# Kernel tuning notes

Hardware: AMD Instinct MI355X
Metric: run time of the kernel (lower is better)

The kernel has to match this reference:

```python
import jax, jax.numpy as jnp
import numpy as np

E = 1024
H = 16
D = E // H
B = 32
S = 1024


def _layernorm(x, gamma, beta, eps=1e-5):
    mu = jnp.mean(x, axis=-1, keepdims=True)
    var = jnp.var(x, axis=-1, keepdims=True)
    return (x - mu) * jax.lax.rsqrt(var + eps) * gamma + beta


def setup_inputs() -> dict:
    key = jax.random.key(0)
    ks = jax.random.split(key, 16)
    w = lambda k, shape: jax.random.normal(k, shape, dtype=jnp.float32) * 0.02
    return {
        "img_feat": jax.random.normal(ks[0], (B, S, E), dtype=jnp.float32),
        "heat_feat": jax.random.normal(ks[1], (B, E), dtype=jnp.float32),
        "W_img": w(ks[2], (E, E)), "b_img": jnp.zeros((E,), jnp.float32),
        "W_heat": w(ks[3], (E, E)), "b_heat": jnp.zeros((E,), jnp.float32),
        "Wq": w(ks[4], (E, E)), "bq": jnp.zeros((E,), jnp.float32),
        "Wk": w(ks[5], (E, E)), "bk": jnp.zeros((E,), jnp.float32),
        "Wv": w(ks[6], (E, E)), "bv": jnp.zeros((E,), jnp.float32),
        "Wo": w(ks[7], (E, E)), "bo": jnp.zeros((E,), jnp.float32),
        "gamma": jnp.ones((E,), jnp.float32),
        "beta": jnp.zeros((E,), jnp.float32),
    }


def reference(img_feat, heat_feat, W_img, b_img, W_heat, b_heat,
              Wq, bq, Wk, bk, Wv, bv, Wo, bo, gamma, beta):
    # projections (torch Linear: x @ W.T + b)
    proj_heat = (heat_feat @ W_heat.T + b_heat)[:, None, :]        # [B,1,E]
    proj_img = img_feat @ W_img.T + b_img                          # [B,S,E]
    # multi-head attention, KV seq len = 1
    q = (proj_img @ Wq.T + bq).reshape(B, S, H, D)
    k = (proj_heat @ Wk.T + bk).reshape(B, 1, H, D)
    v = (proj_heat @ Wv.T + bv).reshape(B, 1, H, D)
    scale = 1.0 / np.sqrt(D).astype(np.float32)
    scores = jnp.einsum('bshd,bthd->bhst', q, k) * scale           # [B,H,S,1]
    attn = jax.nn.softmax(scores, axis=-1)                         # == ones
    ctx = jnp.einsum('bhst,bthd->bshd', attn, v).reshape(B, S, E)
    attn_out = ctx @ Wo.T + bo                                     # [B,S,E]
    # residual + LayerNorm (dropout is identity in eval)
    return _layernorm(img_feat + attn_out, gamma, beta)
```

## Files before the change

kernel.cpp:

```cpp
#include <hip/hip_runtime.h>


#define E_DIM 1024
#define B_DIM 32
#define S_DIM 1024

__global__ __launch_bounds__(256) void gemv_f32(
        const float* __restrict__ W,
        const float* __restrict__ bias,
        const float* __restrict__ x,
        float* __restrict__ y) {
    int wave = threadIdx.x >> 6;
    int lane = threadIdx.x & 63;
    int out_idx = (blockIdx.x << 2) + wave;
    int b = out_idx >> 10;
    int e = out_idx & (E_DIM - 1);
    const float4* w4 = reinterpret_cast<const float4*>(W + (size_t)e * E_DIM);
    const float4* x4 = reinterpret_cast<const float4*>(x + (size_t)b * E_DIM);
    float acc = 0.f;
    #pragma unroll
    for (int p = 0; p < 4; ++p) {
        float4 wv = w4[p * 64 + lane];
        float4 xv = x4[p * 64 + lane];
        acc += wv.x * xv.x + wv.y * xv.y + wv.z * xv.z + wv.w * xv.w;
    }
    #pragma unroll
    for (int off = 32; off; off >>= 1)
        acc += __shfl_down(acc, off, 64);
    if (lane == 0) y[out_idx] = acc + bias[e];
}

__global__ __launch_bounds__(256) void resid_layernorm(
        const float* __restrict__ img,
        const float* __restrict__ a,
        const float* __restrict__ gamma,
        const float* __restrict__ beta,
        float* __restrict__ out) {
    const int row = blockIdx.x;
    const int b = row >> 10;
    const int t = threadIdx.x;

    const float4* imgp = reinterpret_cast<const float4*>(img + (size_t)row * E_DIM);
    const float4* ap   = reinterpret_cast<const float4*>(a + (size_t)b * E_DIM);

    float4 iv = imgp[t];
    float4 av = ap[t];

    float x0 = iv.x + av.x;
    float x1 = iv.y + av.y;
    float x2 = iv.z + av.z;
    float x3 = iv.w + av.w;

    float s = x0 + x1 + x2 + x3;
    float q = x0 * x0 + x1 * x1 + x2 * x2 + x3 * x3;

    #pragma unroll
    for (int off = 32; off; off >>= 1) {
        s += __shfl_down(s, off, 64);
        q += __shfl_down(q, off, 64);
    }

    __shared__ float ssum[4], sqq[4];
    int wv = t >> 6, ln = t & 63;
    if (ln == 0) { ssum[wv] = s; sqq[wv] = q; }
    __syncthreads();
    if (t == 0) {
        float S = ssum[0] + ssum[1] + ssum[2] + ssum[3];
        float Q = sqq[0] + sqq[1] + sqq[2] + sqq[3];
        float mu = S * (1.0f / E_DIM);
        float var = Q * (1.0f / E_DIM) - mu * mu;
        ssum[0] = mu;
        sqq[0] = rsqrtf(var + 1e-5f);
    }
    __syncthreads();
    float mu = ssum[0];
    float rstd = sqq[0];

    const float4* gp = reinterpret_cast<const float4*>(gamma) + t;
    const float4* bp = reinterpret_cast<const float4*>(beta) + t;
    float4 gv = *gp, bv = *bp;

    float4 ov;
    ov.x = (x0 - mu) * rstd * gv.x + bv.x;
    ov.y = (x1 - mu) * rstd * gv.y + bv.y;
    ov.z = (x2 - mu) * rstd * gv.z + bv.z;
    ov.w = (x3 - mu) * rstd * gv.w + bv.w;

    reinterpret_cast<float4*>(out + (size_t)row * E_DIM)[t] = ov;
}

extern "C" void kernel_launch(void* const* d_in, const int* in_sizes, int n_in,
                              void* d_out, int out_size, void* d_ws, size_t ws_size,
                              hipStream_t stream) {
    const float* heat   = (const float*)d_in[1];
    const float* W_heat = (const float*)d_in[4];
    const float* b_heat = (const float*)d_in[5];
    const float* Wv     = (const float*)d_in[10];
    const float* bvv    = (const float*)d_in[11];
    const float* Wo     = (const float*)d_in[12];
    const float* bo     = (const float*)d_in[13];
    const float* img    = (const float*)d_in[0];
    const float* gamma  = (const float*)d_in[14];
    const float* beta   = (const float*)d_in[15];
    float* out = (float*)d_out;

    float* ws = (float*)d_ws;
    float* tt = ws;
    float* vv = ws + B_DIM * E_DIM;
    float* aa = ws + 2 * B_DIM * E_DIM;

    const int n_be = B_DIM * E_DIM;
    const int gemv_blocks = n_be / 4;

    gemv_f32<<<gemv_blocks, 256, 0, stream>>>(W_heat, b_heat, heat, tt);
    gemv_f32<<<gemv_blocks, 256, 0, stream>>>(Wv, bvv, tt, vv);
    gemv_f32<<<gemv_blocks, 256, 0, stream>>>(Wo, bo, vv, aa);

    resid_layernorm<<<B_DIM * S_DIM, 256, 0, stream>>>(img, aa, gamma, beta, out);
}
```

Measured before the change: 295.0 us.

## Reuse weight rows across batches in GEMV and process multiple LayerNorm rows per wave

```diff
diff --git a/kernel.cpp b/kernel.cpp
--- a/kernel.cpp
+++ b/kernel.cpp
@@ -5,88 +5,125 @@
 #define B_DIM 32
 #define S_DIM 1024
 
-__global__ __launch_bounds__(256) void gemv_f32(
+__global__ __launch_bounds__(256) void gemv_xlds(
         const float* __restrict__ W,
         const float* __restrict__ bias,
         const float* __restrict__ x,
         float* __restrict__ y) {
-    int wave = threadIdx.x >> 6;
-    int lane = threadIdx.x & 63;
-    int out_idx = (blockIdx.x << 2) + wave;
-    int b = out_idx >> 10;
-    int e = out_idx & (E_DIM - 1);
+    __shared__ float4 xs[8 * 256];
+    const int t = threadIdx.x;
+    const int rg = blockIdx.x & 255;
+    const int bq = blockIdx.x >> 8;
+
+    const float4* x4 = reinterpret_cast<const float4*>(x) + (size_t)bq * 8 * 256;
+    #pragma unroll
+    for (int i = 0; i < 8; ++i)
+        xs[i * 256 + t] = x4[i * 256 + t];
+    __syncthreads();
+
+    const int wave = t >> 6;
+    const int lane = t & 63;
+    const int e = rg * 4 + wave;
+
     const float4* w4 = reinterpret_cast<const float4*>(W + (size_t)e * E_DIM);
-    const float4* x4 = reinterpret_cast<const float4*>(x + (size_t)b * E_DIM);
-    float acc = 0.f;
+    float4 w0 = w4[lane];
+    float4 w1 = w4[64 + lane];
+    float4 w2 = w4[128 + lane];
+    float4 w3 = w4[192 + lane];
+
+    float acc[8];
     #pragma unroll
-    for (int p = 0; p < 4; ++p) {
-        float4 wv = w4[p * 64 + lane];
-        float4 xv = x4[p * 64 + lane];
-        acc += wv.x * xv.x + wv.y * xv.y + wv.z * xv.z + wv.w * xv.w;
+    for (int i = 0; i < 8; ++i) acc[i] = 0.f;
+
+    #pragma unroll
+    for (int i = 0; i < 8; ++i) {
+        float4 a0 = xs[i * 256 + lane];
+        float4 a1 = xs[i * 256 + 64 + lane];
+        float4 a2 = xs[i * 256 + 128 + lane];
+        float4 a3 = xs[i * 256 + 192 + lane];
+        float r = w0.x * a0.x + w0.y * a0.y + w0.z * a0.z + w0.w * a0.w;
+        r += w1.x * a1.x + w1.y * a1.y + w1.z * a1.z + w1.w * a1.w;
+        r += w2.x * a2.x + w2.y * a2.y + w2.z * a2.z + w2.w * a2.w;
+        r += w3.x * a3.x + w3.y * a3.y + w3.z * a3.z + w3.w * a3.w;
+        acc[i] = r;
     }
+
     #pragma unroll
-    for (int off = 32; off; off >>= 1)
-        acc += __shfl_down(acc, off, 64);
-    if (lane == 0) y[out_idx] = acc + bias[e];
+    for (int off = 32; off; off >>= 1) {
+        #pragma unroll
+        for (int i = 0; i < 8; ++i)
+            acc[i] += __shfl_xor(acc[i], off, 64);
+    }
+
+    if (lane == 0) {
+        const float bs = bias[e];
+        #pragma unroll
+        for (int i = 0; i < 8; ++i)
+            y[(size_t)(bq * 8 + i) * E_DIM + e] = acc[i] + bs;
+    }
 }
 
-__global__ __launch_bounds__(256) void resid_layernorm(
+__global__ __launch_bounds__(256) void resid_ln(
         const float* __restrict__ img,
         const float* __restrict__ a,
         const float* __restrict__ gamma,
         const float* __restrict__ beta,
         float* __restrict__ out) {
-    const int row = blockIdx.x;
-    const int b = row >> 10;
     const int t = threadIdx.x;
+    const int wave = t >> 6;
+    const int lane = t & 63;
+    const int row0 = blockIdx.x * 16 + wave * 4;
+    const int b = row0 >> 10;
 
-    const float4* imgp = reinterpret_cast<const float4*>(img + (size_t)row * E_DIM);
-    const float4* ap   = reinterpret_cast<const float4*>(a + (size_t)b * E_DIM);
-
-    float4 iv = imgp[t];
-    float4 av = ap[t];
-
-    float x0 = iv.x + av.x;
-    float x1 = iv.y + av.y;
-    float x2 = iv.z + av.z;
-    float x3 = iv.w + av.w;
-
-    float s = x0 + x1 + x2 + x3;
-    float q = x0 * x0 + x1 * x1 + x2 * x2 + x3 * x3;
+    const float4* g4  = reinterpret_cast<const float4*>(gamma);
+    const float4* be4 = reinterpret_cast<const float4*>(beta);
+    const float4* a4  = reinterpret_cast<const float4*>(a + (size_t)b * E_DIM);
+    float4 gv[4], bv[4], av[4];
+    #pragma unroll
+    for (int p = 0; p < 4; ++p) {
+        gv[p] = g4[p * 64 + lane];
+        bv[p] = be4[p * 64 + lane];
+        av[p] = a4[p * 64 + lane];
+    }
 
     #pragma unroll
-    for (int off = 32; off; off >>= 1) {
-        s += __shfl_down(s, off, 64);
-        q += __shfl_down(q, off, 64);
+    for (int r = 0; r < 4; ++r) {
+        const size_t base = (size_t)(row0 + r) * E_DIM;
+        const float4* i4 = reinterpret_cast<const float4*>(img + base);
+
+        float4 x[4];
+        float s = 0.f, q = 0.f;
+        #pragma unroll
+        for (int p = 0; p < 4; ++p) {
+            float4 iv = i4[p * 64 + lane];
+            x[p].x = iv.x + av[p].x;
+            x[p].y = iv.y + av[p].y;
+            x[p].z = iv.z + av[p].z;
+            x[p].w = iv.w + av[p].w;
+            s += x[p].x + x[p].y + x[p].z + x[p].w;
+            q += x[p].x * x[p].x + x[p].y * x[p].y
+               + x[p].z * x[p].z + x[p].w * x[p].w;
+        }
+
+        #pragma unroll
+        for (int off = 32; off; off >>= 1) {
+            s += __shfl_xor(s, off, 64);
+            q += __shfl_xor(q, off, 64);
+        }
+        const float mu   = s * (1.0f / E_DIM);
+        const float rstd = rsqrtf(q * (1.0f / E_DIM) - mu * mu + 1e-5f);
+
+        float4* o4 = reinterpret_cast<float4*>(out + base);
+        #pragma unroll
+        for (int p = 0; p < 4; ++p) {
+            float4 ov;
+            ov.x = (x[p].x - mu) * rstd * gv[p].x + bv[p].x;
+            ov.y = (x[p].y - mu) * rstd * gv[p].y + bv[p].y;
+            ov.z = (x[p].z - mu) * rstd * gv[p].z + bv[p].z;
+            ov.w = (x[p].w - mu) * rstd * gv[p].w + bv[p].w;
+            o4[p * 64 + lane] = ov;
+        }
     }
-
-    __shared__ float ssum[4], sqq[4];
-    int wv = t >> 6, ln = t & 63;
-    if (ln == 0) { ssum[wv] = s; sqq[wv] = q; }
-    __syncthreads();
-    if (t == 0) {
-        float S = ssum[0] + ssum[1] + ssum[2] + ssum[3];
-        float Q = sqq[0] + sqq[1] + sqq[2] + sqq[3];
-        float mu = S * (1.0f / E_DIM);
-        float var = Q * (1.0f / E_DIM) - mu * mu;
-        ssum[0] = mu;
-        sqq[0] = rsqrtf(var + 1e-5f);
-    }
-    __syncthreads();
-    float mu = ssum[0];
-    float rstd = sqq[0];
-
-    const float4* gp = reinterpret_cast<const float4*>(gamma) + t;
-    const float4* bp = reinterpret_cast<const float4*>(beta) + t;
-    float4 gv = *gp, bv = *bp;
-
-    float4 ov;
-    ov.x = (x0 - mu) * rstd * gv.x + bv.x;
-    ov.y = (x1 - mu) * rstd * gv.y + bv.y;
-    ov.z = (x2 - mu) * rstd * gv.z + bv.z;
-    ov.w = (x3 - mu) * rstd * gv.w + bv.w;
-
-    reinterpret_cast<float4*>(out + (size_t)row * E_DIM)[t] = ov;
 }
 
 extern "C" void kernel_launch(void* const* d_in, const int* in_sizes, int n_in,
@@ -109,12 +146,9 @@
     float* vv = ws + B_DIM * E_DIM;
     float* aa = ws + 2 * B_DIM * E_DIM;
 
-    const int n_be = B_DIM * E_DIM;
-    const int gemv_blocks = n_be / 4;
+    gemv_xlds<<<1024, 256, 0, stream>>>(W_heat, b_heat, heat, tt);
+    gemv_xlds<<<1024, 256, 0, stream>>>(Wv, bvv, tt, vv);
+    gemv_xlds<<<1024, 256, 0, stream>>>(Wo, bo, vv, aa);
 
-    gemv_f32<<<gemv_blocks, 256, 0, stream>>>(W_heat, b_heat, heat, tt);
-    gemv_f32<<<gemv_blocks, 256, 0, stream>>>(Wv, bvv, tt, vv);
-    gemv_f32<<<gemv_blocks, 256, 0, stream>>>(Wo, bo, vv, aa);
-
-    resid_layernorm<<<B_DIM * S_DIM, 256, 0, stream>>>(img, aa, gamma, beta, out);
+    resid_ln<<<(B_DIM * S_DIM) / 16, 256, 0, stream>>>(img, aa, gamma, beta, out);
 }
```

New measurement: 296.3 us. Within noise of the previous version (+0.4%).
